# Kernel tuning notes

Measured on AMD Instinct MI355X. Metric: run time of the kernel, lower is better.

## Reference

```python
import jax, jax.numpy as jnp
import numpy as np

TEMPERATURE = 0.5
EPS = 1e-8  # torch.nn.CosineSimilarity eps


def setup_inputs() -> dict:
    key = jax.random.key(0)
    k1, k2 = jax.random.split(key)
    B, D = 4096, 128
    z_i = jax.random.normal(k1, (B, D), dtype=jnp.float32)
    z_j = jax.random.normal(k2, (B, D), dtype=jnp.float32)
    return {"z_i": z_i, "z_j": z_j}


def _nt_xent(z_i, z_j, temperature=TEMPERATURE):
    B = z_i.shape[0]
    reps = jnp.concatenate([z_i, z_j], axis=0)                 # [N, D], N = 2B
    norms = jnp.maximum(jnp.linalg.norm(reps, axis=1, keepdims=True), EPS)
    zn = reps / norms                                          # normalize once
    sim = jnp.matmul(zn, zn.T) / temperature                   # [N, N] via GEMM
    exp_sim = jnp.exp(sim)
    # positives: offset-diagonals +B and -B
    idx = jnp.arange(B)
    sim_i_j = exp_sim[idx, idx + B]
    sim_j_i = exp_sim[idx + B, idx]
    pos_pairs = jnp.concatenate([sim_i_j, sim_j_i], axis=0)    # [N]
    sim_self = jnp.diagonal(exp_sim)                           # [N]
    denominator = jnp.sum(exp_sim, axis=1) - sim_self          # [N]
    itemized_loss = -jnp.log(pos_pairs / denominator)
    return jnp.mean(itemized_loss)


def reference(z_i, z_j):
    return _nt_xent(z_i, z_j)
```

## Files before the change

### kernel.cpp

```cpp
#include <hip/hip_runtime.h>
#include <hip/hip_bf16.h>

#define B_ROWS 4096
#define N_ROWS 8192
#define D 128
#define SCALE 2.885390081777927f
#define LN2 0.6931471805599453f

#define RB 256
#define CSPLIT 512
#define CHUNK 64
#define NCHUNK (CSPLIT / CHUNK)

typedef __attribute__((ext_vector_type(8))) short bf16x8;
typedef __attribute__((ext_vector_type(4))) float f32x4;

__device__ inline unsigned short f32_to_bf16_rne(float f) {
    unsigned int u = __float_as_uint(f);
    u += 0x7fffu + ((u >> 16) & 1u);
    return (unsigned short)(u >> 16);
}
__device__ inline float bf16s_to_f32(short s) {
    unsigned int u = ((unsigned int)(unsigned short)s) << 16;
    return __uint_as_float(u);
}

__global__ void k_normalize(const float* __restrict__ z_i,
                            const float* __restrict__ z_j,
                            unsigned short* __restrict__ zn,
                            float* __restrict__ denom,
                            float* __restrict__ out) {
    if (blockIdx.x < 32) denom[blockIdx.x * 256 + threadIdx.x] = 0.f;
    if (blockIdx.x == 0 && threadIdx.x == 0) out[0] = 0.f;

    int row  = blockIdx.x * 4 + (threadIdx.x >> 6);
    int lane = threadIdx.x & 63;
    const float* src = (row < B_ROWS) ? (z_i + (size_t)row * D)
                                      : (z_j + (size_t)(row - B_ROWS) * D);
    float2 v = ((const float2*)src)[lane];
    float ss = v.x * v.x + v.y * v.y;
    #pragma unroll
    for (int m = 1; m < 64; m <<= 1) ss += __shfl_xor(ss, m);
    float rinv = 1.0f / fmaxf(sqrtf(ss), 1e-8f);
    ushort2 o;
    o.x = f32_to_bf16_rne(v.x * rinv);
    o.y = f32_to_bf16_rne(v.y * rinv);
    ((ushort2*)(zn + (size_t)row * D))[lane] = o;
}

__global__ __launch_bounds__(256, 2)
void k_simsum(const unsigned short* __restrict__ zn,
              float* __restrict__ denom) {
    __shared__ unsigned short sB[2 * CHUNK * 16 * 8];
    const int tid  = threadIdx.x;
    const int wave = tid >> 6;
    const int lane = tid & 63;
    const int l15  = lane & 15;
    const int quad = lane >> 4;
    const int m0   = blockIdx.x * RB + wave * 64;

    bf16x8 A[4][4];
    #pragma unroll
    for (int rt = 0; rt < 4; ++rt)
        #pragma unroll
        for (int kb = 0; kb < 4; ++kb)
            A[rt][kb] = *(const bf16x8*)(zn + (size_t)(m0 + rt * 16 + l15) * D + kb * 32 + quad * 8);

    float rs[4][4];
    #pragma unroll
    for (int rt = 0; rt < 4; ++rt)
        #pragma unroll
        for (int j = 0; j < 4; ++j) rs[rt][j] = 0.f;

    const int c_base = blockIdx.y * CSPLIT;

    float4 st[4];
    #pragma unroll
    for (int p = 0; p < 4; ++p) {
        int i = tid + p * 256, c = i >> 4, j = i & 15;
        st[p] = *(const float4*)(zn + (size_t)(c_base + c) * D + j * 8);
    }

    for (int cb = 0; cb < NCHUNK; ++cb) {
        unsigned short* buf = sB + (cb & 1) * (CHUNK * 16 * 8);
        #pragma unroll
        for (int p = 0; p < 4; ++p) {
            int i = tid + p * 256, c = i >> 4, j = i & 15;
            int piece = c * 16 + (j ^ (c & 7));
            *(float4*)(buf + piece * 8) = st[p];
        }
        __syncthreads();

        if (cb + 1 < NCHUNK) {
            #pragma unroll
            for (int p = 0; p < 4; ++p) {
                int i = tid + p * 256, c = i >> 4, j = i & 15;
                st[p] = *(const float4*)(zn + (size_t)(c_base + (cb + 1) * CHUNK + c) * D + j * 8);
            }
        }

        #pragma unroll
        for (int t = 0; t < 4; ++t) {
            bf16x8 b[4];
            #pragma unroll
            for (int kb = 0; kb < 4; ++kb) {
                int c = t * 16 + l15;
                int piece = c * 16 + ((kb * 4 + quad) ^ (c & 7));
                b[kb] = *(const bf16x8*)(buf + piece * 8);
            }
            f32x4 acc[4];
            #pragma unroll
            for (int rt = 0; rt < 4; ++rt) acc[rt] = (f32x4){0.f, 0.f, 0.f, 0.f};
            #pragma unroll
            for (int kb = 0; kb < 4; ++kb)
                #pragma unroll
                for (int rt = 0; rt < 4; ++rt)
                    acc[rt] = __builtin_amdgcn_mfma_f32_16x16x32_bf16(A[rt][kb], b[kb], acc[rt], 0, 0, 0);
            #pragma unroll
            for (int rt = 0; rt < 4; ++rt)
                #pragma unroll
                for (int j = 0; j < 4; ++j)
                    rs[rt][j] += __builtin_amdgcn_exp2f(acc[rt][j] * SCALE);
        }
    }

    #pragma unroll
    for (int rt = 0; rt < 4; ++rt)
        #pragma unroll
        for (int j = 0; j < 4; ++j) {
            float v = rs[rt][j];
            v += __shfl_xor(v, 1);
            v += __shfl_xor(v, 2);
            v += __shfl_xor(v, 4);
            v += __shfl_xor(v, 8);
            rs[rt][j] = v;
        }
    if (l15 == 0) {
        #pragma unroll
        for (int rt = 0; rt < 4; ++rt)
            #pragma unroll
            for (int j = 0; j < 4; ++j)
                atomicAdd(&denom[m0 + rt * 16 + quad * 4 + j], rs[rt][j]);
    }
}

__global__ void k_finalize(const unsigned short* __restrict__ zn,
                           const float* __restrict__ denom,
                           float* __restrict__ out) {
    int i = blockIdx.x * blockDim.x + threadIdx.x;
    int p = (i + B_ROWS) & (N_ROWS - 1);
    const unsigned short* zi = zn + (size_t)i * D;
    const unsigned short* zp = zn + (size_t)p * D;
    float self_dot = 0.f, pos_dot = 0.f;
    #pragma unroll
    for (int c = 0; c < D / 8; ++c) {
        bf16x8 a = *(const bf16x8*)(zi + c * 8);
        bf16x8 b = *(const bf16x8*)(zp + c * 8);
        #pragma unroll
        for (int j = 0; j < 8; ++j) {
            float av = bf16s_to_f32(a[j]);
            float bv = bf16s_to_f32(b[j]);
            self_dot += av * av;
            pos_dot  += av * bv;
        }
    }
    float dnm  = denom[i] - __builtin_amdgcn_exp2f(self_dot * SCALE);
    float loss = __builtin_amdgcn_logf(dnm) * LN2 - pos_dot * 2.0f;

    float v = loss;
    #pragma unroll
    for (int m = 1; m < 64; m <<= 1) v += __shfl_xor(v, m);
    __shared__ float ws[4];
    int wave = threadIdx.x >> 6;
    if ((threadIdx.x & 63) == 0) ws[wave] = v;
    __syncthreads();
    if (threadIdx.x == 0) {
        float s = ws[0] + ws[1] + ws[2] + ws[3];
        atomicAdd(out, s * (1.0f / (float)N_ROWS));
    }
}

extern "C" void kernel_launch(void* const* d_in, const int* in_sizes, int n_in,
                              void* d_out, int out_size, void* d_ws, size_t ws_size,
                              hipStream_t stream) {
    const float* z_i = (const float*)d_in[0];
    const float* z_j = (const float*)d_in[1];
    float* out = (float*)d_out;

    unsigned short* zn = (unsigned short*)d_ws;
    float* denom = (float*)((char*)d_ws + (size_t)N_ROWS * D * 2);

    k_normalize<<<N_ROWS / 4, 256, 0, stream>>>(z_i, z_j, zn, denom, out);
    k_simsum<<<dim3(N_ROWS / RB, N_ROWS / CSPLIT), 256, 0, stream>>>(zn, denom);
    k_finalize<<<N_ROWS / 256, 256, 0, stream>>>(zn, denom, out);
}
```

Baseline: 94.17 us.

## Prescale A operand, drop LDS staging, replace atomics with per-stripe partial sums

The normalize kernel now also writes a copy of the normalized rows pre-multiplied by the exp2 scale, so the GEMM epilogue no longer needs a multiply before exp2. The simsum kernel drops the shared-memory double buffer and its barriers, and each lane loads its B fragments straight from global/L2 with one-tile register prefetch. Row sums are written to per-stripe partial buffers instead of being accumulated with atomics, and the finalize kernel adds them up. This adds an extra bf16 copy of the inputs and makes B loads uncoalesced per lane. Rounding the scaled values to bf16 slightly changes numerics.

Result: slower. 101.3 us (+7.5%).

```diff
diff --git a/kernel.cpp b/kernel.cpp
--- a/kernel.cpp
+++ b/kernel.cpp
@@ -9,8 +9,8 @@
 
 #define RB 256
 #define CSPLIT 512
-#define CHUNK 64
-#define NCHUNK (CSPLIT / CHUNK)
+#define NSTRIPE (N_ROWS / CSPLIT)
+#define NT (CSPLIT / 16)
 
 typedef __attribute__((ext_vector_type(8))) short bf16x8;
 typedef __attribute__((ext_vector_type(4))) float f32x4;
@@ -28,9 +28,8 @@
 __global__ void k_normalize(const float* __restrict__ z_i,
                             const float* __restrict__ z_j,
                             unsigned short* __restrict__ zn,
-                            float* __restrict__ denom,
+                            unsigned short* __restrict__ znA,
                             float* __restrict__ out) {
-    if (blockIdx.x < 32) denom[blockIdx.x * 256 + threadIdx.x] = 0.f;
     if (blockIdx.x == 0 && threadIdx.x == 0) out[0] = 0.f;
 
     int row  = blockIdx.x * 4 + (threadIdx.x >> 6);
@@ -42,16 +41,19 @@
     #pragma unroll
     for (int m = 1; m < 64; m <<= 1) ss += __shfl_xor(ss, m);
     float rinv = 1.0f / fmaxf(sqrtf(ss), 1e-8f);
-    ushort2 o;
-    o.x = f32_to_bf16_rne(v.x * rinv);
-    o.y = f32_to_bf16_rne(v.y * rinv);
-    ((ushort2*)(zn + (size_t)row * D))[lane] = o;
+    ushort2 o, oa;
+    o.x  = f32_to_bf16_rne(v.x * rinv);
+    o.y  = f32_to_bf16_rne(v.y * rinv);
+    oa.x = f32_to_bf16_rne(v.x * rinv * SCALE);
+    oa.y = f32_to_bf16_rne(v.y * rinv * SCALE);
+    ((ushort2*)(zn  + (size_t)row * D))[lane] = o;
+    ((ushort2*)(znA + (size_t)row * D))[lane] = oa;
 }
 
 __global__ __launch_bounds__(256, 2)
 void k_simsum(const unsigned short* __restrict__ zn,
-              float* __restrict__ denom) {
-    __shared__ unsigned short sB[2 * CHUNK * 16 * 8];
+              const unsigned short* __restrict__ znA,
+              float* __restrict__ partial) {
     const int tid  = threadIdx.x;
     const int wave = tid >> 6;
     const int lane = tid & 63;
@@ -64,7 +66,7 @@
     for (int rt = 0; rt < 4; ++rt)
         #pragma unroll
         for (int kb = 0; kb < 4; ++kb)
-            A[rt][kb] = *(const bf16x8*)(zn + (size_t)(m0 + rt * 16 + l15) * D + kb * 32 + quad * 8);
+            A[rt][kb] = *(const bf16x8*)(znA + (size_t)(m0 + rt * 16 + l15) * D + kb * 32 + quad * 8);
 
     float rs[4][4];
     #pragma unroll
@@ -72,55 +74,35 @@
         #pragma unroll
         for (int j = 0; j < 4; ++j) rs[rt][j] = 0.f;
 
-    const int c_base = blockIdx.y * CSPLIT;
+    const unsigned short* bp = zn + (size_t)(blockIdx.y * CSPLIT + l15) * D + quad * 8;
 
-    float4 st[4];
+    bf16x8 bc[4];
     #pragma unroll
-    for (int p = 0; p < 4; ++p) {
-        int i = tid + p * 256, c = i >> 4, j = i & 15;
-        st[p] = *(const float4*)(zn + (size_t)(c_base + c) * D + j * 8);
-    }
+    for (int kb = 0; kb < 4; ++kb) bc[kb] = *(const bf16x8*)(bp + kb * 32);
 
-    for (int cb = 0; cb < NCHUNK; ++cb) {
-        unsigned short* buf = sB + (cb & 1) * (CHUNK * 16 * 8);
+    for (int t = 0; t < NT; ++t) {
+        bf16x8 bn[4];
+        if (t + 1 < NT) {
+            const unsigned short* np = bp + (size_t)(t + 1) * 16 * D;
+            #pragma unroll
+            for (int kb = 0; kb < 4; ++kb) bn[kb] = *(const bf16x8*)(np + kb * 32);
+        }
+        f32x4 acc[4];
         #pragma unroll
-        for (int p = 0; p < 4; ++p) {
-            int i = tid + p * 256, c = i >> 4, j = i & 15;
-            int piece = c * 16 + (j ^ (c & 7));
-            *(float4*)(buf + piece * 8) = st[p];
-        }
-        __syncthreads();
-
-        if (cb + 1 < NCHUNK) {
-            #pragma unroll
-            for (int p = 0; p < 4; ++p) {
-                int i = tid + p * 256, c = i >> 4, j = i & 15;
-                st[p] = *(const float4*)(zn + (size_t)(c_base + (cb + 1) * CHUNK + c) * D + j * 8);
-            }
-        }
-
+        for (int rt = 0; rt < 4; ++rt) acc[rt] = (f32x4){0.f, 0.f, 0.f, 0.f};
         #pragma unroll
-        for (int t = 0; t < 4; ++t) {
-            bf16x8 b[4];
-            #pragma unroll
-            for (int kb = 0; kb < 4; ++kb) {
-                int c = t * 16 + l15;
-                int piece = c * 16 + ((kb * 4 + quad) ^ (c & 7));
-                b[kb] = *(const bf16x8*)(buf + piece * 8);
-            }
-            f32x4 acc[4];
-            #pragma unroll
-            for (int rt = 0; rt < 4; ++rt) acc[rt] = (f32x4){0.f, 0.f, 0.f, 0.f};
-            #pragma unroll
-            for (int kb = 0; kb < 4; ++kb)
-                #pragma unroll
-                for (int rt = 0; rt < 4; ++rt)
-                    acc[rt] = __builtin_amdgcn_mfma_f32_16x16x32_bf16(A[rt][kb], b[kb], acc[rt], 0, 0, 0);
+        for (int kb = 0; kb < 4; ++kb)
             #pragma unroll
             for (int rt = 0; rt < 4; ++rt)
-                #pragma unroll
-                for (int j = 0; j < 4; ++j)
-                    rs[rt][j] += __builtin_amdgcn_exp2f(acc[rt][j] * SCALE);
+                acc[rt] = __builtin_amdgcn_mfma_f32_16x16x32_bf16(A[rt][kb], bc[kb], acc[rt], 0, 0, 0);
+        #pragma unroll
+        for (int rt = 0; rt < 4; ++rt)
+            #pragma unroll
+            for (int j = 0; j < 4; ++j)
+                rs[rt][j] += __builtin_amdgcn_exp2f(acc[rt][j]);
+        if (t + 1 < NT) {
+            #pragma unroll
+            for (int kb = 0; kb < 4; ++kb) bc[kb] = bn[kb];
         }
     }
 
@@ -136,36 +118,45 @@
             rs[rt][j] = v;
         }
     if (l15 == 0) {
+        float* dst = partial + (size_t)blockIdx.y * N_ROWS;
         #pragma unroll
         for (int rt = 0; rt < 4; ++rt)
             #pragma unroll
             for (int j = 0; j < 4; ++j)
-                atomicAdd(&denom[m0 + rt * 16 + quad * 4 + j], rs[rt][j]);
+                dst[m0 + rt * 16 + quad * 4 + j] = rs[rt][j];
     }
 }
 
 __global__ void k_finalize(const unsigned short* __restrict__ zn,
-                           const float* __restrict__ denom,
+                           const unsigned short* __restrict__ znA,
+                           const float* __restrict__ partial,
                            float* __restrict__ out) {
     int i = blockIdx.x * blockDim.x + threadIdx.x;
     int p = (i + B_ROWS) & (N_ROWS - 1);
-    const unsigned short* zi = zn + (size_t)i * D;
-    const unsigned short* zp = zn + (size_t)p * D;
-    float self_dot = 0.f, pos_dot = 0.f;
+
+    float dsum = 0.f;
+    #pragma unroll
+    for (int s = 0; s < NSTRIPE; ++s)
+        dsum += partial[(size_t)s * N_ROWS + i];
+
+    const unsigned short* ai  = znA + (size_t)i * D;
+    const unsigned short* bi  = zn  + (size_t)i * D;
+    const unsigned short* bpp = zn  + (size_t)p * D;
+    float self_l2 = 0.f, pos_l2 = 0.f;
     #pragma unroll
     for (int c = 0; c < D / 8; ++c) {
-        bf16x8 a = *(const bf16x8*)(zi + c * 8);
-        bf16x8 b = *(const bf16x8*)(zp + c * 8);
+        bf16x8 a = *(const bf16x8*)(ai  + c * 8);
+        bf16x8 s = *(const bf16x8*)(bi  + c * 8);
+        bf16x8 q = *(const bf16x8*)(bpp + c * 8);
         #pragma unroll
         for (int j = 0; j < 8; ++j) {
             float av = bf16s_to_f32(a[j]);
-            float bv = bf16s_to_f32(b[j]);
-            self_dot += av * av;
-            pos_dot  += av * bv;
+            self_l2 += av * bf16s_to_f32(s[j]);
+            pos_l2  += av * bf16s_to_f32(q[j]);
         }
     }
-    float dnm  = denom[i] - __builtin_amdgcn_exp2f(self_dot * SCALE);
-    float loss = __builtin_amdgcn_logf(dnm) * LN2 - pos_dot * 2.0f;
+    float dnm  = dsum - __builtin_amdgcn_exp2f(self_l2);
+    float loss = (__builtin_amdgcn_logf(dnm) - pos_l2) * LN2;
 
     float v = loss;
     #pragma unroll
@@ -175,8 +166,8 @@
     if ((threadIdx.x & 63) == 0) ws[wave] = v;
     __syncthreads();
     if (threadIdx.x == 0) {
-        float s = ws[0] + ws[1] + ws[2] + ws[3];
-        atomicAdd(out, s * (1.0f / (float)N_ROWS));
+        float sm = ws[0] + ws[1] + ws[2] + ws[3];
+        atomicAdd(out, sm * (1.0f / (float)N_ROWS));
     }
 }
 
@@ -187,10 +178,12 @@
     const float* z_j = (const float*)d_in[1];
     float* out = (float*)d_out;
 
-    unsigned short* zn = (unsigned short*)d_ws;
-    float* denom = (float*)((char*)d_ws + (size_t)N_ROWS * D * 2);
+    char* ws = (char*)d_ws;
+    unsigned short* zn      = (unsigned short*)ws;
+    unsigned short* znA     = (unsigned short*)(ws + (size_t)N_ROWS * D * 2);
+    float*          partial = (float*)(ws + (size_t)N_ROWS * D * 4);
 
-    k_normalize<<<N_ROWS / 4, 256, 0, stream>>>(z_i, z_j, zn, denom, out);
-    k_simsum<<<dim3(N_ROWS / RB, N_ROWS / CSPLIT), 256, 0, stream>>>(zn, denom);
-    k_finalize<<<N_ROWS / 256, 256, 0, stream>>>(zn, denom, out);
+    k_normalize<<<N_ROWS / 4, 256, 0, stream>>>(z_i, z_j, zn, znA, out);
+    k_simsum<<<dim3(N_ROWS / RB, NSTRIPE), 256, 0, stream>>>(zn, znA, partial);
+    k_finalize<<<N_ROWS / 256, 256, 0, stream>>>(zn, znA, partial, out);
 }
```
